# Optimization experiments

Measured on AMD Instinct MI355X. Metric: run time of the kernel, lower is better.

## Reference

```python
import jax, jax.numpy as jnp
import numpy as np

HEADS = 8
DIM_HEAD = 64
ROPE_THETA = 10000.0


def _rope(t):
    # t: [b, h, n, d]; interleaved-pair rotation as in rotary-embedding-torch
    n, d = t.shape[-2], t.shape[-1]
    inv_freq = 1.0 / (ROPE_THETA ** (jnp.arange(0, d, 2, dtype=jnp.float32) / d))  # [d/2]
    freqs = jnp.arange(n, dtype=jnp.float32)[:, None] * inv_freq[None, :]  # [n, d/2]
    freqs = jnp.repeat(freqs, 2, axis=-1)  # [n, d], repeated per pair
    cos, sin = jnp.cos(freqs), jnp.sin(freqs)
    x1 = t[..., 0::2]
    x2 = t[..., 1::2]
    rot = jnp.stack((-x2, x1), axis=-1).reshape(t.shape)  # rotate_half
    return t * cos + rot * sin


def setup_inputs() -> dict:
    key = jax.random.key(0)
    k1, k2, k3, k4 = jax.random.split(key, 4)
    b, n, dim = 2, 2048, 512
    hidden = HEADS * DIM_HEAD
    x = jax.random.normal(k1, (b, n, dim), dtype=jnp.float32)
    pos_bias = jax.random.normal(k2, (HEADS, n, n), dtype=jnp.float32) * 0.02
    w_qkv = jax.random.normal(k3, (dim, 3 * hidden), dtype=jnp.float32) * (dim ** -0.5)
    w_out = jax.random.normal(k4, (hidden, dim), dtype=jnp.float32) * (hidden ** -0.5)
    return {"x": x, "pos_bias": pos_bias, "w_qkv": w_qkv, "w_out": w_out}


def reference(x, pos_bias, w_qkv, w_out):
    b, n, _ = x.shape
    qkv = x @ w_qkv  # [b, n, 3*hidden]
    q, k, v = jnp.split(qkv, 3, axis=-1)

    def to_heads(t):
        return t.reshape(b, n, HEADS, DIM_HEAD).transpose(0, 2, 1, 3)  # [b,h,n,d]

    q, k, v = map(to_heads, (q, k, v))
    k = _rope(k)
    q = _rope(q * (DIM_HEAD ** -0.5))
    sim = jnp.einsum('bhid,bhjd->bhij', q, k)  # [b,h,n,n]
    sim = sim + pos_bias  # broadcast over batch
    sim = sim - jax.lax.stop_gradient(jnp.max(sim, axis=-1, keepdims=True))
    attn = jax.nn.softmax(sim, axis=-1)
    out = jnp.einsum('bhij,bhjd->bhid', attn, v)
    out = out.transpose(0, 2, 1, 3).reshape(b, n, HEADS * DIM_HEAD)
    return out @ w_out
```

## Files before the change

kernel.cpp:

```cpp
#include <hip/hip_runtime.h>
#include <math.h>

#define SEQ 2048
#define NHEAD 8
#define HDIM 64
#define BATCH 2

typedef __attribute__((ext_vector_type(8))) short short8;
typedef __attribute__((ext_vector_type(4))) float f32x4;

__device__ __forceinline__ ushort f2bf(float f) {
    union { float f; unsigned u; } v; v.f = f;
    unsigned r = v.u + 0x7FFFu + ((v.u >> 16) & 1u);
    return (ushort)(r >> 16);
}

__device__ __forceinline__ f32x4 mfma16(short8 a, short8 b, f32x4 c) {
    return __builtin_amdgcn_mfma_f32_16x16x32_bf16(a, b, c, 0, 0, 0);
}

__device__ __forceinline__ void gld16(const void* g, void* l) {
    __builtin_amdgcn_global_load_lds(
        (const __attribute__((address_space(1))) unsigned int*)g,
        (__attribute__((address_space(3))) unsigned int*)l, 16, 0, 0);
}

__global__ __launch_bounds__(256)
void prep(const float* __restrict__ x, const float* __restrict__ w_qkv,
          const float* __restrict__ w_out, ushort* __restrict__ xb,
          ushort* __restrict__ wqkvT, ushort* __restrict__ woutT)
{
    __shared__ ushort tile[64][66];
    const int blk = blockIdx.x, t = threadIdx.x;
    if (blk < 1024) {
        const int i = (blk * 256 + t) * 8;
        float4 a = *(const float4*)&x[i];
        float4 b = *(const float4*)&x[i + 4];
        union { ushort us[8]; uint4 v; } pk;
        pk.us[0] = f2bf(a.x); pk.us[1] = f2bf(a.y); pk.us[2] = f2bf(a.z); pk.us[3] = f2bf(a.w);
        pk.us[4] = f2bf(b.x); pk.us[5] = f2bf(b.y); pk.us[6] = f2bf(b.z); pk.us[7] = f2bf(b.w);
        *(uint4*)&xb[i] = pk.v;
        return;
    }
    const float* w; ushort* wT; int K, N, n0, k0;
    if (blk < 1216) { const int s = blk - 1024; w = w_qkv; wT = wqkvT; K = 512; N = 1536; n0 = (s % 24) * 64; k0 = (s / 24) * 64; }
    else            { const int s = blk - 1216; w = w_out; wT = woutT; K = 512; N = 512;  n0 = (s % 8) * 64;  k0 = (s / 8) * 64; }
#pragma unroll
    for (int i = 0; i < 4; ++i) {
        const int slot = t + i * 256;
        const int r = slot >> 4, c4 = (slot & 15) * 4;
        float4 v = *(const float4*)&w[(size_t)(k0 + r) * N + n0 + c4];
        tile[c4 + 0][r] = f2bf(v.x);
        tile[c4 + 1][r] = f2bf(v.y);
        tile[c4 + 2][r] = f2bf(v.z);
        tile[c4 + 3][r] = f2bf(v.w);
    }
    __syncthreads();
    const int n = t >> 2, kc = (t & 3) * 16;
    union { ushort us[16]; uint4 v[2]; } o;
#pragma unroll
    for (int j = 0; j < 16; ++j) o.us[j] = tile[n][kc + j];
    *(uint4*)&wT[(size_t)(n0 + n) * K + k0 + kc]     = o.v[0];
    *(uint4*)&wT[(size_t)(n0 + n) * K + k0 + kc + 8] = o.v[1];
}

__global__ __launch_bounds__(256)
void gemm_qkv_rope(const ushort* __restrict__ xb, const ushort* __restrict__ wT,
                   ushort* __restrict__ qb, ushort* __restrict__ kb,
                   ushort* __restrict__ vtb)
{
    __shared__ __align__(16) ushort As[64][64];
    __shared__ __align__(16) ushort Bs[128][64];
    const int t = threadIdx.x, lane = t & 63, w = t >> 6;
    const int quad = lane >> 4, l16 = lane & 15;
    const int m0 = blockIdx.y * 64, n0 = blockIdx.x * 128;
    const int mw = (w >> 1) * 32, nw = (w & 1) * 64;
    const int krow = lane >> 3, kcol = (lane & 7) * 8;
    f32x4 acc[2][4] = {};

    for (int k0 = 0; k0 < 512; k0 += 64) {
        __syncthreads();
        gld16(&xb[(size_t)(m0 + w * 8 + krow) * 512 + k0 + kcol],        &As[w * 8][0]);
        gld16(&xb[(size_t)(m0 + (w + 4) * 8 + krow) * 512 + k0 + kcol],  &As[(w + 4) * 8][0]);
#pragma unroll
        for (int jj = 0; jj < 4; ++jj) {
            const int j = w * 4 + jj;
            gld16(&wT[(size_t)(n0 + j * 8 + krow) * 512 + k0 + kcol], &Bs[j * 8][0]);
        }
        __syncthreads();
#pragma unroll
        for (int ks = 0; ks < 2; ++ks) {
            short8 a[2], b[4];
#pragma unroll
            for (int i = 0; i < 2; ++i)
                a[i] = *(const short8*)&As[mw + i * 16 + l16][ks * 32 + quad * 8];
#pragma unroll
            for (int j = 0; j < 4; ++j)
                b[j] = *(const short8*)&Bs[nw + j * 16 + l16][ks * 32 + quad * 8];
#pragma unroll
            for (int i = 0; i < 2; ++i)
#pragma unroll
                for (int j = 0; j < 4; ++j)
                    acc[i][j] = mfma16(a[i], b[j], acc[i][j]);
        }
    }

    const int sec = (n0 + nw) >> 9;
    if (sec == 2) {
#pragma unroll
        for (int i = 0; i < 2; ++i) {
            const int m = m0 + mw + i * 16 + quad * 4;
            const int bidx = m >> 11, n = m & 2047;
#pragma unroll
            for (int j = 0; j < 4; ++j) {
                const int nc = n0 + nw + j * 16 + l16;
                const int d = nc & 63, h = (nc >> 6) & 7;
                ushort4 pk;
                pk.x = f2bf(acc[i][j][0]); pk.y = f2bf(acc[i][j][1]);
                pk.z = f2bf(acc[i][j][2]); pk.w = f2bf(acc[i][j][3]);
                *(ushort4*)&vtb[(((size_t)bidx * 8 + h) * 64 + d) * 2048 + n] = pk;
            }
        }
    } else {
        ushort* dst = (sec == 0) ? qb : kb;
        const float scale = (sec == 0) ? 0.125f : 1.0f;
#pragma unroll
        for (int j = 0; j < 4; ++j) {
            const int nc = n0 + nw + j * 16 + l16;
            const int d = nc & 63, h = (nc >> 6) & 7;
            const float inv = __expf(-(float)(d & ~1) * (9.2103403719761836f / 64.0f));
#pragma unroll
            for (int i = 0; i < 2; ++i)
#pragma unroll
            for (int r = 0; r < 4; ++r) {
                const int m = m0 + mw + i * 16 + quad * 4 + r;
                const int bidx = m >> 11, n = m & 2047;
                float sn, cs;
                __sincosf((float)n * inv, &sn, &cs);
                const float vacc = acc[i][j][r];
                const float partner = __shfl_xor(vacc, 1);
                const float rot = (d & 1) ? (vacc * cs + partner * sn)
                                          : (vacc * cs - partner * sn);
                dst[(((size_t)bidx * 8 + h) * 2048 + n) * 64 + d] = f2bf(rot * scale);
            }
        }
    }
}

__global__ __launch_bounds__(256)
void flash_attn_mfma(const ushort* __restrict__ qb, const ushort* __restrict__ kb,
                     const ushort* __restrict__ vtb, const float* __restrict__ bias,
                     ushort* __restrict__ ob)
{
    __shared__ __align__(16) ushort Ks[64][64];
    __shared__ __align__(16) ushort Vt[64][64];
    __shared__ __align__(16) float  Bl[64][64];
    __shared__ __align__(16) ushort Ps[4][16][72];
    const int t = threadIdx.x, lane = t & 63, w = t >> 6;
    const int quad = lane >> 4, l16 = lane & 15;
    const int q0 = blockIdx.x * 64, h = blockIdx.y, b = blockIdx.z;
    const size_t bh = (size_t)(b * NHEAD + h);
    const ushort* Q  = qb  + bh * SEQ * HDIM;
    const ushort* Kp = kb  + bh * SEQ * HDIM;
    const ushort* VT = vtb + bh * HDIM * SEQ;

    short8 qf[2];
    qf[0] = *(const short8*)&Q[(size_t)(q0 + w * 16 + l16) * HDIM + quad * 8];
    qf[1] = *(const short8*)&Q[(size_t)(q0 + w * 16 + l16) * HDIM + 32 + quad * 8];

    f32x4 oacc[4] = {};
    float lsum[4] = {};
    const int krow = lane >> 3, kcol = (lane & 7) * 8;
    const int brow = lane >> 4, bcol = (lane & 15) * 4;

    for (int it = 0; it < 32; ++it) {
        const int k0 = it * 64;
        __syncthreads();
        gld16(&Kp[(size_t)(k0 + w * 8 + krow) * HDIM + kcol],       &Ks[w * 8][0]);
        gld16(&Kp[(size_t)(k0 + (w + 4) * 8 + krow) * HDIM + kcol], &Ks[(w + 4) * 8][0]);
        gld16(&VT[(size_t)(w * 8 + krow) * SEQ + k0 + kcol],        &Vt[w * 8][0]);
        gld16(&VT[(size_t)((w + 4) * 8 + krow) * SEQ + k0 + kcol],  &Vt[(w + 4) * 8][0]);
#pragma unroll
        for (int jj = 0; jj < 4; ++jj) {
            const int j = w * 4 + jj;
            gld16(&bias[((size_t)h * SEQ + q0 + j * 4 + brow) * SEQ + k0 + bcol], &Bl[j * 4][0]);
        }
        __syncthreads();

        f32x4 sacc[4] = {};
#pragma unroll
        for (int ks = 0; ks < 2; ++ks)
#pragma unroll
            for (int s = 0; s < 4; ++s) {
                short8 kf = *(const short8*)&Ks[s * 16 + l16][ks * 32 + quad * 8];
                sacc[s] = mfma16(qf[ks], kf, sacc[s]);
            }

#pragma unroll
        for (int r = 0; r < 4; ++r)
#pragma unroll
            for (int s = 0; s < 4; ++s) {
                const float p = __expf(sacc[s][r] + Bl[w * 16 + quad * 4 + r][s * 16 + l16]);
                lsum[r] += p;
                Ps[w][quad * 4 + r][s * 16 + l16] = f2bf(p);
            }
        asm volatile("" ::: "memory");

#pragma unroll
        for (int ks = 0; ks < 2; ++ks) {
            short8 pf = *(const short8*)&Ps[w][l16][ks * 32 + quad * 8];
#pragma unroll
            for (int s = 0; s < 4; ++s) {
                short8 vf = *(const short8*)&Vt[s * 16 + l16][ks * 32 + quad * 8];
                oacc[s] = mfma16(pf, vf, oacc[s]);
            }
        }
    }

#pragma unroll
    for (int r = 0; r < 4; ++r) {
        float rs = lsum[r];
        rs += __shfl_xor(rs, 1, 16);
        rs += __shfl_xor(rs, 2, 16);
        rs += __shfl_xor(rs, 4, 16);
        rs += __shfl_xor(rs, 8, 16);
        const float invl = 1.0f / rs;
        const size_t m = (size_t)b * SEQ + q0 + w * 16 + quad * 4 + r;
#pragma unroll
        for (int s = 0; s < 4; ++s)
            ob[m * 512 + h * HDIM + s * 16 + l16] = f2bf(oacc[s][r] * invl);
    }
}

__global__ __launch_bounds__(256)
void gemm_out(const ushort* __restrict__ Ab, const ushort* __restrict__ wT,
              float* __restrict__ C)
{
    __shared__ __align__(16) ushort As[64][64];
    __shared__ __align__(16) ushort Bs[64][64];
    const int t = threadIdx.x, lane = t & 63, w = t >> 6;
    const int quad = lane >> 4, l16 = lane & 15;
    const int m0 = blockIdx.y * 64, n0 = blockIdx.x * 64;
    const int mw = (w >> 1) * 32, nw = (w & 1) * 32;
    const int krow = lane >> 3, kcol = (lane & 7) * 8;
    f32x4 acc[2][2] = {};

    for (int k0 = 0; k0 < 512; k0 += 64) {
        __syncthreads();
        gld16(&Ab[(size_t)(m0 + w * 8 + krow) * 512 + k0 + kcol],       &As[w * 8][0]);
        gld16(&Ab[(size_t)(m0 + (w + 4) * 8 + krow) * 512 + k0 + kcol], &As[(w + 4) * 8][0]);
        gld16(&wT[(size_t)(n0 + w * 8 + krow) * 512 + k0 + kcol],       &Bs[w * 8][0]);
        gld16(&wT[(size_t)(n0 + (w + 4) * 8 + krow) * 512 + k0 + kcol], &Bs[(w + 4) * 8][0]);
        __syncthreads();
#pragma unroll
        for (int ks = 0; ks < 2; ++ks) {
            short8 a[2], b[2];
#pragma unroll
            for (int i = 0; i < 2; ++i)
                a[i] = *(const short8*)&As[mw + i * 16 + l16][ks * 32 + quad * 8];
#pragma unroll
            for (int j = 0; j < 2; ++j)
                b[j] = *(const short8*)&Bs[nw + j * 16 + l16][ks * 32 + quad * 8];
#pragma unroll
            for (int i = 0; i < 2; ++i)
#pragma unroll
                for (int j = 0; j < 2; ++j)
                    acc[i][j] = mfma16(a[i], b[j], acc[i][j]);
        }
    }
#pragma unroll
    for (int i = 0; i < 2; ++i)
#pragma unroll
    for (int r = 0; r < 4; ++r) {
        const int m = m0 + mw + i * 16 + quad * 4 + r;
#pragma unroll
        for (int j = 0; j < 2; ++j)
            C[(size_t)m * 512 + n0 + nw + j * 16 + l16] = acc[i][j][r];
    }
}

extern "C" void kernel_launch(void* const* d_in, const int* in_sizes, int n_in,
                              void* d_out, int out_size, void* d_ws, size_t ws_size,
                              hipStream_t stream)
{
    const float* x        = (const float*)d_in[0];
    const float* pos_bias = (const float*)d_in[1];
    const float* w_qkv    = (const float*)d_in[2];
    const float* w_out    = (const float*)d_in[3];
    float* out = (float*)d_out;

    char* ws = (char*)d_ws;
    ushort* xb     = (ushort*)(ws);
    ushort* wqkvT  = (ushort*)(ws + 4194304);
    ushort* woutT  = (ushort*)(ws + 5767168);
    ushort* qb     = (ushort*)(ws + 6291456);
    ushort* kb     = (ushort*)(ws + 10485760);
    ushort* vtb    = (ushort*)(ws + 14680064);
    ushort* attnb  = (ushort*)(ws + 18874368);

    prep<<<1280, 256, 0, stream>>>(x, w_qkv, w_out, xb, wqkvT, woutT);
    gemm_qkv_rope<<<dim3(12, 64), 256, 0, stream>>>(xb, wqkvT, qb, kb, vtb);
    flash_attn_mfma<<<dim3(SEQ / 64, NHEAD, BATCH), 256, 0, stream>>>(qb, kb, vtb, pos_bias, attnb);
    gemm_out<<<dim3(8, 64), 256, 0, stream>>>(attnb, woutT, out);
}
```

Measured before the change: 257.6 us.

## Double-buffer K/V/bias tiles and XOR-swizzle LDS layout in flash attention

The attention kernel now keeps two LDS buffers for the K, V^T and bias tiles. The next tile is loaded asynchronously while the current one is computed, and the loop needs only one barrier per iteration. The K and V^T tiles are also stored with an XOR swizzle on 16-byte chunks to reduce LDS bank conflicts on the MFMA operand reads. LDS use roughly doubles, to about 50KB per block, which may lower occupancy. Correctness now depends on the global_load_lds writes being complete before the barrier waits.

Measured after the change: 257.4 us. About the same (-0.1%).

```diff
diff --git a/kernel.cpp b/kernel.cpp
--- a/kernel.cpp
+++ b/kernel.cpp
@@ -152,9 +152,9 @@
                      const ushort* __restrict__ vtb, const float* __restrict__ bias,
                      ushort* __restrict__ ob)
 {
-    __shared__ __align__(16) ushort Ks[64][64];
-    __shared__ __align__(16) ushort Vt[64][64];
-    __shared__ __align__(16) float  Bl[64][64];
+    __shared__ __align__(16) ushort Ks[2][64][64];
+    __shared__ __align__(16) ushort Vt[2][64][64];
+    __shared__ __align__(16) float  Bl[2][64][64];
     __shared__ __align__(16) ushort Ps[4][16][72];
     const int t = threadIdx.x, lane = t & 63, w = t >> 6;
     const int quad = lane >> 4, l16 = lane & 15;
@@ -170,37 +170,48 @@
 
     f32x4 oacc[4] = {};
     float lsum[4] = {};
-    const int krow = lane >> 3, kcol = (lane & 7) * 8;
+    const int krow = lane >> 3;
+    const int kcolsw = ((lane & 7) ^ krow) * 8;
     const int brow = lane >> 4, bcol = (lane & 15) * 4;
 
-    for (int it = 0; it < 32; ++it) {
-        const int k0 = it * 64;
-        __syncthreads();
-        gld16(&Kp[(size_t)(k0 + w * 8 + krow) * HDIM + kcol],       &Ks[w * 8][0]);
-        gld16(&Kp[(size_t)(k0 + (w + 4) * 8 + krow) * HDIM + kcol], &Ks[(w + 4) * 8][0]);
-        gld16(&VT[(size_t)(w * 8 + krow) * SEQ + k0 + kcol],        &Vt[w * 8][0]);
-        gld16(&VT[(size_t)((w + 4) * 8 + krow) * SEQ + k0 + kcol],  &Vt[(w + 4) * 8][0]);
+    const int sw = l16 & 7;
+    const int c0 = (quad ^ sw) * 8;
+    const int c1 = ((quad + 4) ^ sw) * 8;
+
+    auto stage = [&](int buf, int it_) {
+        const int k0 = it_ * 64;
+        gld16(&Kp[(size_t)(k0 + w * 8 + krow) * HDIM + kcolsw],       &Ks[buf][w * 8][0]);
+        gld16(&Kp[(size_t)(k0 + (w + 4) * 8 + krow) * HDIM + kcolsw], &Ks[buf][(w + 4) * 8][0]);
+        gld16(&VT[(size_t)(w * 8 + krow) * SEQ + k0 + kcolsw],        &Vt[buf][w * 8][0]);
+        gld16(&VT[(size_t)((w + 4) * 8 + krow) * SEQ + k0 + kcolsw],  &Vt[buf][(w + 4) * 8][0]);
 #pragma unroll
         for (int jj = 0; jj < 4; ++jj) {
             const int j = w * 4 + jj;
-            gld16(&bias[((size_t)h * SEQ + q0 + j * 4 + brow) * SEQ + k0 + bcol], &Bl[j * 4][0]);
-        }
-        __syncthreads();
+            gld16(&bias[((size_t)h * SEQ + q0 + j * 4 + brow) * SEQ + k0 + bcol], &Bl[buf][j * 4][0]);
+        }
+    };
+
+    stage(0, 0);
+    __syncthreads();
+
+    for (int it = 0; it < 32; ++it) {
+        const int cur = it & 1;
+        if (it + 1 < 32) stage(cur ^ 1, it + 1);
 
         f32x4 sacc[4] = {};
 #pragma unroll
-        for (int ks = 0; ks < 2; ++ks)
+        for (int s = 0; s < 4; ++s) {
+            short8 kf0 = *(const short8*)&Ks[cur][s * 16 + l16][c0];
+            sacc[s] = mfma16(qf[0], kf0, sacc[s]);
+            short8 kf1 = *(const short8*)&Ks[cur][s * 16 + l16][c1];
+            sacc[s] = mfma16(qf[1], kf1, sacc[s]);
+        }
+
+#pragma unroll
+        for (int r = 0; r < 4; ++r)
 #pragma unroll
             for (int s = 0; s < 4; ++s) {
-                short8 kf = *(const short8*)&Ks[s * 16 + l16][ks * 32 + quad * 8];
-                sacc[s] = mfma16(qf[ks], kf, sacc[s]);
-            }
-
-#pragma unroll
-        for (int r = 0; r < 4; ++r)
-#pragma unroll
-            for (int s = 0; s < 4; ++s) {
-                const float p = __expf(sacc[s][r] + Bl[w * 16 + quad * 4 + r][s * 16 + l16]);
+                const float p = __expf(sacc[s][r] + Bl[cur][w * 16 + quad * 4 + r][s * 16 + l16]);
                 lsum[r] += p;
                 Ps[w][quad * 4 + r][s * 16 + l16] = f2bf(p);
             }
@@ -209,12 +220,15 @@
 #pragma unroll
         for (int ks = 0; ks < 2; ++ks) {
             short8 pf = *(const short8*)&Ps[w][l16][ks * 32 + quad * 8];
+            const int cc = ks ? c1 : c0;
 #pragma unroll
             for (int s = 0; s < 4; ++s) {
-                short8 vf = *(const short8*)&Vt[s * 16 + l16][ks * 32 + quad * 8];
+                short8 vf = *(const short8*)&Vt[cur][s * 16 + l16][cc];
                 oacc[s] = mfma16(pf, vf, oacc[s]);
             }
         }
+
+        __syncthreads();
     }
 
 #pragma unroll
```
